# Optimization experiments

Measured on AMD Instinct MI355X. Metric: run time of the kernel, lower is better.

The kernel has to match this reference:

```python
import jax, jax.numpy as jnp
from jax import lax
import numpy as np

EPS = 1e-5


def setup_inputs() -> dict:
    key = jax.random.key(0)
    ks = jax.random.split(key, 16)
    N, C, H, W = 8, 128, 128, 128
    MIP, OUP, K = 8, 128, 3
    inp = {}
    inp["x"] = jax.random.normal(ks[0], (N, C, H, W), dtype=jnp.float32)
    # conv1: 1x1, C -> MIP
    inp["w1"] = jax.random.normal(ks[1], (MIP, C), dtype=jnp.float32) * (1.0 / np.sqrt(C))
    inp["b1"] = jax.random.normal(ks[2], (MIP,), dtype=jnp.float32) * 0.02
    # bn1 (inference: frozen running stats)
    inp["g1"] = jnp.ones((MIP,), jnp.float32) + jax.random.normal(ks[3], (MIP,), jnp.float32) * 0.02
    inp["be1"] = jax.random.normal(ks[4], (MIP,), jnp.float32) * 0.02
    inp["m1"] = jax.random.normal(ks[5], (MIP,), jnp.float32) * 0.02
    inp["v1"] = jnp.ones((MIP,), jnp.float32)
    # conv_h / conv_w: 1x1, MIP -> C
    inp["wh"] = jax.random.normal(ks[6], (C, MIP), dtype=jnp.float32) * (1.0 / np.sqrt(MIP))
    inp["bh"] = jax.random.normal(ks[7], (C,), dtype=jnp.float32) * 0.02
    inp["ww"] = jax.random.normal(ks[8], (C, MIP), dtype=jnp.float32) * (1.0 / np.sqrt(MIP))
    inp["bw"] = jax.random.normal(ks[9], (C,), dtype=jnp.float32) * 0.02
    # final conv: KxK, C -> OUP
    inp["wc"] = jax.random.normal(ks[10], (OUP, C, K, K), dtype=jnp.float32) * (1.0 / np.sqrt(C * K * K))
    inp["bc"] = jax.random.normal(ks[11], (OUP,), dtype=jnp.float32) * 0.02
    inp["g2"] = jnp.ones((OUP,), jnp.float32) + jax.random.normal(ks[12], (OUP,), jnp.float32) * 0.02
    inp["be2"] = jax.random.normal(ks[13], (OUP,), jnp.float32) * 0.02
    inp["m2"] = jax.random.normal(ks[14], (OUP,), jnp.float32) * 0.02
    inp["v2"] = jnp.ones((OUP,), jnp.float32)
    return inp


def _bn1d(y, g, b, m, v):
    # y: (n, c, l); per-channel affine with frozen stats
    s = g / jnp.sqrt(v + EPS)
    return y * s[None, :, None] + (b - m * s)[None, :, None]


def _h_swish(y):
    return y * jnp.clip(y + 3.0, 0.0, 6.0) / 6.0


def reference(x, w1, b1, g1, be1, m1, v1, wh, bh, ww, bw, wc, bc, g2, be2, m2, v2):
    n, c, h, w = x.shape
    # Multi-scale pooled descriptors. Nearest interp of the 2-bin and 4-bin
    # adaptive pools back to length-1 picks bin 0, i.e. the mean over the
    # first half / first quarter of the pooled axis.
    x_h = x.mean(3) + x[..., : w // 2].mean(3) + x[..., : w // 4].mean(3)        # (n,c,h)
    x_w = x.mean(2) + x[:, :, : h // 2].mean(2) + x[:, :, : h // 4].mean(2)      # (n,c,w)
    y = jnp.concatenate([x_h, x_w], axis=2)                                       # (n,c,h+w)
    y = jnp.einsum('ncl,mc->nml', y, w1) + b1[None, :, None]                      # 1x1 conv
    y = _h_swish(_bn1d(y, g1, be1, m1, v1))
    xh, xw = y[:, :, :h], y[:, :, h:]
    a_h = jax.nn.sigmoid(jnp.einsum('nml,cm->ncl', xh, wh) + bh[None, :, None])[:, :, :, None]  # (n,c,h,1)
    a_w = jax.nn.sigmoid(jnp.einsum('nml,cm->ncl', xw, ww) + bw[None, :, None])[:, :, None, :]  # (n,c,1,w)
    out = x * a_w * a_h                                                           # gated features
    # final conv (kernel 3, stride 1, pad 1) + BN + SiLU
    out = lax.conv_general_dilated(out, wc, window_strides=(1, 1),
                                   padding=[(1, 1), (1, 1)],
                                   dimension_numbers=('NCHW', 'OIHW', 'NCHW'))
    out = out + bc[None, :, None, None]
    s2 = g2 / jnp.sqrt(v2 + EPS)
    out = out * s2[None, :, None, None] + (be2 - m2 * s2)[None, :, None, None]
    return out * jax.nn.sigmoid(out)
```

## Files before the change

### kernel.cpp

```cpp
#include <hip/hip_runtime.h>
#include <hip/hip_bf16.h>

typedef float f32x4 __attribute__((ext_vector_type(4)));
typedef __bf16 bf16x8 __attribute__((ext_vector_type(8)));

#define EPSF 1e-5f

__device__ __forceinline__ float pw(int i) {
    return (1.0f + (i < 64 ? 2.0f : 0.0f) + (i < 32 ? 4.0f : 0.0f)) * (1.0f / 128.0f);
}

__global__ __launch_bounds__(256) void pool_kernel(const float* __restrict__ x,
                                                   float* __restrict__ P) {
    int nc = blockIdx.x;
    const f32x4* plane = (const f32x4*)(x + (size_t)nc * 16384);
    __shared__ float rowpart[128][33];
    __shared__ __align__(16) f32x4 colpart[8][32];
    int t = threadIdx.x;
    int wq = t & 31, hg = t >> 5;
    f32x4 cacc = {0.f, 0.f, 0.f, 0.f};
    float u0 = pw(wq * 4), u1 = pw(wq * 4 + 1), u2 = pw(wq * 4 + 2), u3 = pw(wq * 4 + 3);
    #pragma unroll
    for (int j = 0; j < 16; ++j) {
        int r = hg * 16 + j;
        f32x4 v = plane[r * 32 + wq];
        rowpart[r][wq] = v.x * u0 + v.y * u1 + v.z * u2 + v.w * u3;
        cacc += v * pw(r);
    }
    colpart[hg][wq] = cacc;
    __syncthreads();
    float s = 0.f;
    if (t < 128) {
        #pragma unroll
        for (int q = 0; q < 32; ++q) s += rowpart[t][q];
        P[(size_t)nc * 256 + t] = s;
    } else {
        int w = t - 128;
        const float* cp = (const float*)colpart;
        #pragma unroll
        for (int g = 0; g < 8; ++g) s += cp[g * 128 + w];
        P[(size_t)nc * 256 + 128 + w] = s;
    }
}

__global__ __launch_bounds__(256) void attn_kernel(const float* __restrict__ P,
    const float* __restrict__ w1, const float* __restrict__ b1,
    const float* __restrict__ g1, const float* __restrict__ be1,
    const float* __restrict__ m1, const float* __restrict__ v1,
    const float* __restrict__ wh, const float* __restrict__ bh,
    const float* __restrict__ ww, const float* __restrict__ bw,
    float* __restrict__ A2) {
    int n = blockIdx.x >> 2, cg = blockIdx.x & 3, t = threadIdx.x;
    __shared__ float w1s[1024], whs[256], wws[256];
    __shared__ float bhs[32], bws[32];
    __shared__ float s1[8], t1[8], b1s[8];
    for (int i = t; i < 1024; i += 256) w1s[i] = w1[i];
    whs[t] = wh[cg * 256 + t];
    wws[t] = ww[cg * 256 + t];
    if (t < 32) { bhs[t] = bh[cg * 32 + t]; bws[t] = bw[cg * 32 + t]; }
    if (t < 8) {
        float s = g1[t] * rsqrtf(v1[t] + EPSF);
        s1[t] = s; t1[t] = be1[t] - m1[t] * s; b1s[t] = b1[t];
    }
    __syncthreads();
    float y[8];
    #pragma unroll
    for (int m = 0; m < 8; ++m) y[m] = b1s[m];
    const float* Pn = P + (size_t)n * 32768;
    for (int c = 0; c < 128; ++c) {
        float pv = Pn[c * 256 + t];
        #pragma unroll
        for (int m = 0; m < 8; ++m) y[m] += w1s[m * 128 + c] * pv;
    }
    #pragma unroll
    for (int m = 0; m < 8; ++m) {
        float v = y[m] * s1[m] + t1[m];
        float cl = fminf(fmaxf(v + 3.f, 0.f), 6.f);
        y[m] = v * cl * (1.f / 6.f);
    }
    const float* Ws_ = (t < 128) ? whs : wws;
    const float* Bs = (t < 128) ? bhs : bws;
    float* On = A2 + (size_t)n * 32768;
    for (int cc = 0; cc < 32; ++cc) {
        int c = cg * 32 + cc;
        float a = Bs[cc];
        #pragma unroll
        for (int m = 0; m < 8; ++m) a += y[m] * Ws_[cc * 8 + m];
        On[c * 256 + t] = 1.f / (1.f + __expf(-a));
    }
}

__global__ __launch_bounds__(256) void wtrans_kernel(const float* __restrict__ wc,
    const float* __restrict__ bc, const float* __restrict__ g2, const float* __restrict__ be2,
    const float* __restrict__ m2, const float* __restrict__ v2,
    __hip_bfloat16* __restrict__ Wt, float* __restrict__ ab) {
    int g = blockIdx.x * 256 + threadIdx.x;
    int step = g >> 12, rem = g & 4095;
    int o = rem >> 5, m = rem & 31;
    int slotp = m >> 3, j = m & 7;
    int u = slotp ^ ((o >> 1) & 3);
    int kidx = u * 8 + j;
    int khw = step >> 2, c32 = step & 3;
    int c = c32 * 32 + kidx;
    Wt[g] = __float2bfloat16(wc[(o * 128 + c) * 9 + khw]);
    if (g < 128) {
        float s2 = g2[g] * rsqrtf(v2[g] + EPSF);
        ab[g] = s2;
        ab[128 + g] = bc[g] * s2 + be2[g] - m2[g] * s2;
    }
}

__device__ __forceinline__ int ldsoff(int w, int c) {
    return w * 128 + ((((c >> 3) ^ ((w & 7) << 1)) << 3) | (c & 7));
}

__global__ __launch_bounds__(256) void amul_kernel(const float* __restrict__ x,
    const float* __restrict__ A2, __hip_bfloat16* __restrict__ Xpad) {
    int nh = blockIdx.x;
    int n = nh >> 7, h = nh & 127;
    int t = threadIdx.x;
    __shared__ __align__(16) __hip_bfloat16 T[16384];
    __shared__ float ahs[128];
    if (t < 128) ahs[t] = A2[(size_t)(n * 128 + t) * 256 + h];

    uint4 z = {0u, 0u, 0u, 0u};
    __hip_bfloat16* Xn = Xpad + (size_t)n * 16900 * 128;
    if (t < 32) {
        int wp = (t & 1) ? 129 : 0, cb2 = t >> 1;
        *(uint4*)(Xn + (size_t)((h + 1) * 130 + wp) * 128 + cb2 * 8) = z;
    }
    if (h == 0 || h == 127) {
        int hp = (h == 0) ? 0 : 129;
        for (int i = t; i < 2080; i += 256) {
            int wp = i >> 4, cb2 = i & 15;
            *(uint4*)(Xn + (size_t)(hp * 130 + wp) * 128 + cb2 * 8) = z;
        }
    }
    __syncthreads();

    const float* xr  = x + ((size_t)n * 128 * 128 + h) * 128;
    const float* awr = A2 + (size_t)n * 32768 + 128;
    #pragma unroll
    for (int j = 0; j < 16; ++j) {
        int item = j * 256 + t;
        int c = item >> 5, w4 = item & 31;
        f32x4 xv = *(const f32x4*)(xr + (size_t)c * 16384 + w4 * 4);
        f32x4 av = *(const f32x4*)(awr + c * 256 + w4 * 4);
        float ah = ahs[c];
        #pragma unroll
        for (int k = 0; k < 4; ++k) {
            float val = xv[k] * av[k] * ah;
            T[ldsoff(w4 * 4 + k, c)] = __float2bfloat16(val);
        }
    }
    __syncthreads();
    __hip_bfloat16* orow = Xn + (size_t)((h + 1) * 130 + 1) * 128;
    #pragma unroll
    for (int j = 0; j < 8; ++j) {
        int item = j * 256 + t;
        int w = item >> 4, cb = item & 15;
        int slot = cb ^ ((w & 7) << 1);
        uint4 v = *(const uint4*)&T[w * 128 + slot * 8];
        *(uint4*)(orow + w * 128 + cb * 8) = v;
    }
}

__global__ __launch_bounds__(512, 4) void conv_kernel(
    const __hip_bfloat16* __restrict__ Xpad, const __hip_bfloat16* __restrict__ Wt,
    const float* __restrict__ ab, float* __restrict__ out) {
    int bid = blockIdx.x;
    int work = (bid & 7) * 64 + (bid >> 3);
    int n = work >> 6, h0 = (work & 63) * 2;
    int tid = threadIdx.x;
    int lane = tid & 63, wid = tid >> 6;
    int wm = wid >> 2, wn = wid & 3;
    int r16 = lane & 15, u = lane >> 4;

    __shared__ __align__(16) __hip_bfloat16 Ws[3 * 4096];
    __shared__ __align__(16) __hip_bfloat16 Xs[3 * 8192];

    const __hip_bfloat16* Xn = Xpad + ((size_t)n * 16900 + (size_t)h0 * 130) * 128;

    int offA[4], offB[4];
    #pragma unroll
    for (int mi = 0; mi < 4; ++mi) {
        int o = wm * 64 + mi * 16 + r16;
        offA[mi] = o * 32 + ((u ^ ((o >> 1) & 3)) << 3);
    }
    #pragma unroll
    for (int ni = 0; ni < 4; ++ni) {
        int p = wn * 64 + ni * 16 + r16;
        offB[ni] = p * 32 + ((u ^ ((p >> 1) & 3)) << 3);
    }

    int xo[2];
    #pragma unroll
    for (int j = 0; j < 2; ++j) {
        int idx = j * 512 + tid, p = idx >> 2, s = idx & 3;
        int r2 = p >> 7, w = p & 127;
        xo[j] = (r2 * 130 + w) * 128 + ((s ^ ((p >> 1) & 3)) << 3);
    }

    auto stage = [&](int t) {
        int khw = t >> 2, c32 = t & 3;
        int kh = khw / 3, kw = khw - kh * 3;
        __builtin_amdgcn_global_load_lds(
            (const __attribute__((address_space(1))) void*)(Wt + t * 4096 + tid * 8),
            (__attribute__((address_space(3))) void*)(&Ws[(t % 3) * 4096 + tid * 8]),
            16, 0, 0);
        const __hip_bfloat16* xsrc = Xn + (kh * 130 + kw) * 128 + c32 * 32;
        __hip_bfloat16* xdst = &Xs[(t % 3) * 8192];
        #pragma unroll
        for (int j = 0; j < 2; ++j)
            __builtin_amdgcn_global_load_lds(
                (const __attribute__((address_space(1))) void*)(xsrc + xo[j]),
                (__attribute__((address_space(3))) void*)(xdst + (j * 512 + tid) * 8),
                16, 0, 0);
    };

    f32x4 acc[4][4];
    #pragma unroll
    for (int i = 0; i < 4; ++i)
        #pragma unroll
        for (int j = 0; j < 4; ++j) acc[i][j] = (f32x4){0.f, 0.f, 0.f, 0.f};

    stage(0);
    stage(1);
    asm volatile("s_waitcnt vmcnt(0)" ::: "memory");
    __builtin_amdgcn_sched_barrier(0);
    __builtin_amdgcn_s_barrier();
    __builtin_amdgcn_sched_barrier(0);

    bf16x8 fa[4], fb[2][4];
    #pragma unroll
    for (int ni = 0; ni < 4; ++ni) fb[0][ni] = *(const bf16x8*)&Xs[offB[ni]];
    __builtin_amdgcn_sched_barrier(0);

    #pragma unroll
    for (int t = 0; t < 36; ++t) {
        const __hip_bfloat16* Wb = &Ws[(t % 3) * 4096];
        const __hip_bfloat16* Xr1 = &Xs[((t + 1) % 3) * 8192];

        if (t + 2 < 36) stage(t + 2);

        #pragma unroll
        for (int mi = 0; mi < 4; ++mi) fa[mi] = *(const bf16x8*)&Wb[offA[mi]];
        __builtin_amdgcn_sched_barrier(0);
        if (t + 1 < 36) {
            #pragma unroll
            for (int ni = 0; ni < 4; ++ni)
                fb[(t + 1) & 1][ni] = *(const bf16x8*)&Xr1[offB[ni]];
            __builtin_amdgcn_sched_barrier(0);
            asm volatile("s_waitcnt lgkmcnt(4)" ::: "memory");
        } else {
            asm volatile("s_waitcnt lgkmcnt(0)" ::: "memory");
        }
        __builtin_amdgcn_sched_barrier(0);

        __builtin_amdgcn_s_setprio(1);
        #pragma unroll
        for (int mi = 0; mi < 4; ++mi)
            #pragma unroll
            for (int ni = 0; ni < 4; ++ni)
                acc[mi][ni] = __builtin_amdgcn_mfma_f32_16x16x32_bf16(
                    fa[mi], fb[t & 1][ni], acc[mi][ni], 0, 0, 0);
        __builtin_amdgcn_s_setprio(0);

        if (t < 35) {
            asm volatile("s_waitcnt lgkmcnt(0)" ::: "memory");
            asm volatile("s_waitcnt vmcnt(0)" ::: "memory");
            __builtin_amdgcn_sched_barrier(0);
            __builtin_amdgcn_s_barrier();
            __builtin_amdgcn_sched_barrier(0);
        }
    }

    #pragma unroll
    for (int mi = 0; mi < 4; ++mi) {
        #pragma unroll
        for (int r = 0; r < 4; ++r) {
            int o = wm * 64 + mi * 16 + u * 4 + r;
            float al = ab[o], be = ab[128 + o];
            size_t obase = (((size_t)n * 128 + o) * 128 + h0) * 128;
            #pragma unroll
            for (int ni = 0; ni < 4; ++ni) {
                int p = wn * 64 + ni * 16 + r16;
                int r2 = p >> 7, w = p & 127;
                float z = acc[mi][ni][r] * al + be;
                out[obase + r2 * 128 + w] = z / (1.f + __expf(-z));
            }
        }
    }
}

extern "C" void kernel_launch(void* const* d_in, const int* in_sizes, int n_in,
                              void* d_out, int out_size, void* d_ws, size_t ws_size,
                              hipStream_t stream) {
    const float* x   = (const float*)d_in[0];
    const float* w1  = (const float*)d_in[1];
    const float* b1  = (const float*)d_in[2];
    const float* g1  = (const float*)d_in[3];
    const float* be1 = (const float*)d_in[4];
    const float* m1  = (const float*)d_in[5];
    const float* v1  = (const float*)d_in[6];
    const float* wh  = (const float*)d_in[7];
    const float* bh  = (const float*)d_in[8];
    const float* ww  = (const float*)d_in[9];
    const float* bw  = (const float*)d_in[10];
    const float* wc  = (const float*)d_in[11];
    const float* bc  = (const float*)d_in[12];
    const float* g2  = (const float*)d_in[13];
    const float* be2 = (const float*)d_in[14];
    const float* m2  = (const float*)d_in[15];
    const float* v2  = (const float*)d_in[16];
    float* out = (float*)d_out;

    char* ws = (char*)d_ws;
    float* P  = (float*)(ws);
    float* A2 = (float*)(ws + (1 << 20));
    __hip_bfloat16* Xpad = (__hip_bfloat16*)(ws + (2 << 20));
    __hip_bfloat16* Wt   = (__hip_bfloat16*)(ws + (2 << 20) + 34611200);
    float* ab = (float*)(ws + (2 << 20) + 34611200 + 294912);

    pool_kernel<<<1024, 256, 0, stream>>>(x, P);
    attn_kernel<<<32, 256, 0, stream>>>(P, w1, b1, g1, be1, m1, v1, wh, bh, ww, bw, A2);
    wtrans_kernel<<<576, 256, 0, stream>>>(wc, bc, g2, be2, m2, v2, Wt, ab);
    amul_kernel<<<1024, 256, 0, stream>>>(x, A2, Xpad);
    conv_kernel<<<512, 512, 0, stream>>>(Xpad, Wt, ab, out);
}
```

Before: 111.0 us.

## Load conv activation fragments directly from global memory, skipping LDS staging

Measured after the change: 151.6 us. +36.5%, slower.

```diff
diff --git a/kernel.cpp b/kernel.cpp
--- a/kernel.cpp
+++ b/kernel.cpp
@@ -165,56 +165,38 @@
     }
 }
 
-__global__ __launch_bounds__(512, 4) void conv_kernel(
+__global__ __launch_bounds__(256, 3) void conv_kernel(
     const __hip_bfloat16* __restrict__ Xpad, const __hip_bfloat16* __restrict__ Wt,
     const float* __restrict__ ab, float* __restrict__ out) {
     int bid = blockIdx.x;
-    int work = (bid & 7) * 64 + (bid >> 3);
-    int n = work >> 6, h0 = (work & 63) * 2;
+    int work = (bid & 7) * 128 + (bid >> 3);
+    int n = work >> 7, h = work & 127;
     int tid = threadIdx.x;
     int lane = tid & 63, wid = tid >> 6;
-    int wm = wid >> 2, wn = wid & 3;
+    int wm = wid >> 1, wn = wid & 1;
     int r16 = lane & 15, u = lane >> 4;
 
     __shared__ __align__(16) __hip_bfloat16 Ws[3 * 4096];
-    __shared__ __align__(16) __hip_bfloat16 Xs[3 * 8192];
-
-    const __hip_bfloat16* Xn = Xpad + ((size_t)n * 16900 + (size_t)h0 * 130) * 128;
-
-    int offA[4], offB[4];
+
+    const __hip_bfloat16* Xn = Xpad + ((size_t)n * 16900 + (size_t)h * 130) * 128;
+
+    int offA[4];
     #pragma unroll
     for (int mi = 0; mi < 4; ++mi) {
         int o = wm * 64 + mi * 16 + r16;
         offA[mi] = o * 32 + ((u ^ ((o >> 1) & 3)) << 3);
     }
-    #pragma unroll
-    for (int ni = 0; ni < 4; ++ni) {
-        int p = wn * 64 + ni * 16 + r16;
-        offB[ni] = p * 32 + ((u ^ ((p >> 1) & 3)) << 3);
-    }
-
-    int xo[2];
-    #pragma unroll
-    for (int j = 0; j < 2; ++j) {
-        int idx = j * 512 + tid, p = idx >> 2, s = idx & 3;
-        int r2 = p >> 7, w = p & 127;
-        xo[j] = (r2 * 130 + w) * 128 + ((s ^ ((p >> 1) & 3)) << 3);
-    }
-
-    auto stage = [&](int t) {
-        int khw = t >> 2, c32 = t & 3;
-        int kh = khw / 3, kw = khw - kh * 3;
-        __builtin_amdgcn_global_load_lds(
-            (const __attribute__((address_space(1))) void*)(Wt + t * 4096 + tid * 8),
-            (__attribute__((address_space(3))) void*)(&Ws[(t % 3) * 4096 + tid * 8]),
-            16, 0, 0);
-        const __hip_bfloat16* xsrc = Xn + (kh * 130 + kw) * 128 + c32 * 32;
-        __hip_bfloat16* xdst = &Xs[(t % 3) * 8192];
+    const __hip_bfloat16* xb[4];
+    #pragma unroll
+    for (int ni = 0; ni < 4; ++ni)
+        xb[ni] = Xn + (wn * 64 + ni * 16 + r16) * 128 + u * 8;
+
+    auto stageW = [&](int t) {
         #pragma unroll
         for (int j = 0; j < 2; ++j)
             __builtin_amdgcn_global_load_lds(
-                (const __attribute__((address_space(1))) void*)(xsrc + xo[j]),
-                (__attribute__((address_space(3))) void*)(xdst + (j * 512 + tid) * 8),
+                (const __attribute__((address_space(1))) void*)(Wt + t * 4096 + (j * 256 + tid) * 8),
+                (__attribute__((address_space(3))) void*)(&Ws[(t % 3) * 4096 + (j * 256 + tid) * 8]),
                 16, 0, 0);
     };
 
@@ -224,37 +206,30 @@
         #pragma unroll
         for (int j = 0; j < 4; ++j) acc[i][j] = (f32x4){0.f, 0.f, 0.f, 0.f};
 
-    stage(0);
-    stage(1);
-    asm volatile("s_waitcnt vmcnt(0)" ::: "memory");
+    bf16x8 fa[4], fb[4];
+
+    stageW(0);
+    stageW(1);
+    #pragma unroll
+    for (int ni = 0; ni < 4; ++ni) fb[ni] = *(const bf16x8*)(xb[ni]);
+    asm volatile("s_waitcnt vmcnt(6)" ::: "memory");
     __builtin_amdgcn_sched_barrier(0);
     __builtin_amdgcn_s_barrier();
     __builtin_amdgcn_sched_barrier(0);
 
-    bf16x8 fa[4], fb[2][4];
-    #pragma unroll
-    for (int ni = 0; ni < 4; ++ni) fb[0][ni] = *(const bf16x8*)&Xs[offB[ni]];
-    __builtin_amdgcn_sched_barrier(0);
-
     #pragma unroll
     for (int t = 0; t < 36; ++t) {
-        const __hip_bfloat16* Wb = &Ws[(t % 3) * 4096];
-        const __hip_bfloat16* Xr1 = &Xs[((t + 1) % 3) * 8192];
-
-        if (t + 2 < 36) stage(t + 2);
-
-        #pragma unroll
-        for (int mi = 0; mi < 4; ++mi) fa[mi] = *(const bf16x8*)&Wb[offA[mi]];
+        if (t + 2 < 36) stageW(t + 2);
+        #pragma unroll
+        for (int mi = 0; mi < 4; ++mi)
+            fa[mi] = *(const bf16x8*)&Ws[(t % 3) * 4096 + offA[mi]];
         __builtin_amdgcn_sched_barrier(0);
-        if (t + 1 < 36) {
-            #pragma unroll
-            for (int ni = 0; ni < 4; ++ni)
-                fb[(t + 1) & 1][ni] = *(const bf16x8*)&Xr1[offB[ni]];
-            __builtin_amdgcn_sched_barrier(0);
-            asm volatile("s_waitcnt lgkmcnt(4)" ::: "memory");
+        if (t + 2 < 36) {
+            asm volatile("s_waitcnt vmcnt(2)" ::: "memory");
         } else {
-            asm volatile("s_waitcnt lgkmcnt(0)" ::: "memory");
-        }
+            asm volatile("s_waitcnt vmcnt(0)" ::: "memory");
+        }
+        asm volatile("s_waitcnt lgkmcnt(0)" ::: "memory");
         __builtin_amdgcn_sched_barrier(0);
 
         __builtin_amdgcn_s_setprio(1);
@@ -263,13 +238,21 @@
             #pragma unroll
             for (int ni = 0; ni < 4; ++ni)
                 acc[mi][ni] = __builtin_amdgcn_mfma_f32_16x16x32_bf16(
-                    fa[mi], fb[t & 1][ni], acc[mi][ni], 0, 0, 0);
+                    fa[mi], fb[ni], acc[mi][ni], 0, 0, 0);
         __builtin_amdgcn_s_setprio(0);
-
+        __builtin_amdgcn_sched_barrier(0);
+
+        if (t + 1 < 36) {
+            const int t1 = t + 1;
+            const int khw = t1 >> 2, c32 = t1 & 3;
+            const int kh = khw / 3, kw = khw - kh * 3;
+            const int sd = (kh * 130 + kw) * 128 + c32 * 32;
+            #pragma unroll
+            for (int ni = 0; ni < 4; ++ni)
+                fb[ni] = *(const bf16x8*)(xb[ni] + sd);
+            __builtin_amdgcn_sched_barrier(0);
+        }
         if (t < 35) {
-            asm volatile("s_waitcnt lgkmcnt(0)" ::: "memory");
-            asm volatile("s_waitcnt vmcnt(0)" ::: "memory");
-            __builtin_amdgcn_sched_barrier(0);
             __builtin_amdgcn_s_barrier();
             __builtin_amdgcn_sched_barrier(0);
         }
@@ -281,13 +264,12 @@
         for (int r = 0; r < 4; ++r) {
             int o = wm * 64 + mi * 16 + u * 4 + r;
             float al = ab[o], be = ab[128 + o];
-            size_t obase = (((size_t)n * 128 + o) * 128 + h0) * 128;
+            size_t obase = (((size_t)n * 128 + o) * 128 + h) * 128;
             #pragma unroll
             for (int ni = 0; ni < 4; ++ni) {
                 int p = wn * 64 + ni * 16 + r16;
-                int r2 = p >> 7, w = p & 127;
                 float z = acc[mi][ni][r] * al + be;
-                out[obase + r2 * 128 + w] = z / (1.f + __expf(-z));
+                out[obase + p] = z / (1.f + __expf(-z));
             }
         }
     }
@@ -326,5 +308,5 @@
     attn_kernel<<<32, 256, 0, stream>>>(P, w1, b1, g1, be1, m1, v1, wh, bh, ww, bw, A2);
     wtrans_kernel<<<576, 256, 0, stream>>>(wc, bc, g2, be2, m2, v2, Wt, ab);
     amul_kernel<<<1024, 256, 0, stream>>>(x, A2, Xpad);
-    conv_kernel<<<512, 512, 0, stream>>>(Xpad, Wt, ab, out);
-}
+    conv_kernel<<<1024, 256, 0, stream>>>(Xpad, Wt, ab, out);
+}
```
